# Optimization experiments

Measured on AMD Instinct MI355X. Metric: run time of the kernel, lower is better.

Reference implementation:

```python
import jax, jax.numpy as jnp
import numpy as np

D = 1024
H = 16
HD = D // H
S = 2048
B = 2
FF = 4 * D
EPS = 1e-5
NEG_INF = -100000.0


def setup_inputs() -> dict:
    key = jax.random.key(0)
    ks = jax.random.split(key, 16)
    sd = 0.02
    inp = {
        'x': jax.random.normal(ks[0], (B, S, D), dtype=jnp.float32),
        'Wq': jax.random.normal(ks[1], (D, D), dtype=jnp.float32) * sd,
        'bq': jnp.zeros((D,), jnp.float32),
        'Wk': jax.random.normal(ks[2], (D, D), dtype=jnp.float32) * sd,
        'bk': jnp.zeros((D,), jnp.float32),
        'Wv': jax.random.normal(ks[3], (D, D), dtype=jnp.float32) * sd,
        'bv': jnp.zeros((D,), jnp.float32),
        'Wo': jax.random.normal(ks[4], (D, D), dtype=jnp.float32) * sd,
        'bo': jnp.zeros((D,), jnp.float32),
        'W1': jax.random.normal(ks[5], (D, FF), dtype=jnp.float32) * sd,
        'b1': jnp.zeros((FF,), jnp.float32),
        'W2': jax.random.normal(ks[6], (FF, D), dtype=jnp.float32) * sd,
        'b2': jnp.zeros((D,), jnp.float32),
        'g1': jnp.ones((D,), jnp.float32),
        's1': jnp.zeros((D,), jnp.float32),
        'g2': jnp.ones((D,), jnp.float32),
        's2': jnp.zeros((D,), jnp.float32),
    }
    return inp


def layer_norm(x, scale, shift):
    # torch: (x - mean) / (std + eps), std with Bessel correction (ddof=1)
    mean = jnp.mean(x, axis=-1, keepdims=True)
    std = jnp.std(x, axis=-1, keepdims=True, ddof=1)
    return (x - mean) / (std + EPS) * scale + shift


def attention(x, Wq, bq, Wk, bk, Wv, bv, Wo, bo):
    b, s, d = x.shape
    q = (x @ Wq + bq).reshape(b, s, H, HD).transpose(0, 2, 1, 3)  # [b,h,s,hd]
    k = (x @ Wk + bk).reshape(b, s, H, HD).transpose(0, 2, 1, 3)
    v = (x @ Wv + bv).reshape(b, s, H, HD).transpose(0, 2, 1, 3)
    scores = jnp.einsum('bhqd,bhkd->bhqk', q, k) / jnp.sqrt(jnp.float32(HD))
    mask = jnp.triu(jnp.ones((s, s), bool), k=1)
    scores = jnp.where(mask, NEG_INF, scores)
    attn = jax.nn.softmax(scores, axis=-1)
    ctx = jnp.einsum('bhqk,bhkd->bhqd', attn, v)
    ctx = ctx.transpose(0, 2, 1, 3).reshape(b, s, d)
    return ctx @ Wo + bo


def reference(x, Wq, bq, Wk, bk, Wv, bv, Wo, bo, W1, b1, W2, b2, g1, s1, g2, s2):
    shortcut = x
    h = layer_norm(x, g1, s1)
    h = attention(h, Wq, bq, Wk, bk, Wv, bv, Wo, bo)
    x = shortcut + h  # dropout=0.0 -> identity
    shortcut = x
    h = layer_norm(x, g2, s2)
    h = jax.nn.gelu(h @ W1 + b1, approximate=False) @ W2 + b2
    return h + shortcut
```

## Files before the change

kernel.cpp:

```cpp
#include <hip/hip_runtime.h>
#include <hip/hip_bf16.h>
#include <math.h>

#define D_   1024
#define H_   16
#define HD_  64
#define S_   2048
#define B_   2
#define FF_  4096
#define M_   (B_*S_)
#define QKVN (3*D_)

typedef __bf16 bf16;
typedef bf16 bf16x8 __attribute__((ext_vector_type(8)));
typedef bf16 bf16x4 __attribute__((ext_vector_type(4)));
typedef float f32x4 __attribute__((ext_vector_type(4)));

#define MFMA16(a,b,c) __builtin_amdgcn_mfma_f32_16x16x32_bf16(a,b,c,0,0,0)

__device__ __forceinline__ void gld16(const void* g, void* l) {
    __builtin_amdgcn_global_load_lds(
        (const __attribute__((address_space(1))) void*)g,
        (__attribute__((address_space(3))) void*)l, 16, 0, 0);
}

__global__ __launch_bounds__(256) void transpose_cast(const float* __restrict__ W,
                                                      bf16* __restrict__ WT,
                                                      int K, int N) {
    __shared__ float t[64][65];
    int k0 = blockIdx.x * 64, n0 = blockIdx.y * 64;
    int tid = threadIdx.x;
    int tr = tid >> 4, tc = tid & 15;
    #pragma unroll
    for (int i = 0; i < 4; i++) {
        int r = tr + i * 16;
        float4 v = *(const float4*)&W[(size_t)(k0 + r) * N + n0 + tc * 4];
        t[r][tc * 4 + 0] = v.x; t[r][tc * 4 + 1] = v.y;
        t[r][tc * 4 + 2] = v.z; t[r][tc * 4 + 3] = v.w;
    }
    __syncthreads();
    #pragma unroll
    for (int i = 0; i < 4; i++) {
        int r = tr + i * 16;
        bf16x4 o;
        #pragma unroll
        for (int j = 0; j < 4; j++) o[j] = (bf16)t[tc * 4 + j][r];
        *(bf16x4*)&WT[(size_t)(n0 + r) * K + k0 + tc * 4] = o;
    }
}

__global__ __launch_bounds__(256) void transpose_v(const bf16* __restrict__ qkv,
                                                   bf16* __restrict__ VT) {
    __shared__ __align__(16) bf16 t[64][72];
    int bh = blockIdx.y; int b = bh >> 4, h = bh & 15;
    int s0 = blockIdx.x * 64;
    const bf16* vbase = qkv + (size_t)b * S_ * QKVN + 2048 + h * 64;
    int tid = threadIdx.x;
    #pragma unroll
    for (int i = 0; i < 2; i++) {
        int e = tid + i * 256; int r = e >> 3, cg = e & 7;
        *(bf16x8*)&t[r][cg * 8] = *(const bf16x8*)&vbase[(size_t)(s0 + r) * QKVN + cg * 8];
    }
    __syncthreads();
    #pragma unroll
    for (int i = 0; i < 2; i++) {
        int e = tid + i * 256; int d = e >> 3, cg = e & 7;
        bf16x8 v;
        #pragma unroll
        for (int j = 0; j < 8; j++) v[j] = t[cg * 8 + j][d];
        *(bf16x8*)&VT[((size_t)bh * 64 + d) * S_ + s0 + cg * 8] = v;
    }
}

__global__ void concat3(const float* __restrict__ a, const float* __restrict__ b,
                        const float* __restrict__ c, float* __restrict__ o) {
    int i = blockIdx.x * 256 + threadIdx.x;
    o[i] = (i < 1024) ? a[i] : (i < 2048 ? b[i - 1024] : c[i - 2048]);
}

__global__ __launch_bounds__(256) void ln_kernel(const float* __restrict__ x,
                                                 const float* __restrict__ g,
                                                 const float* __restrict__ sh,
                                                 bf16* __restrict__ out) {
    int row = blockIdx.x * 4 + (threadIdx.x >> 6);
    int lane = threadIdx.x & 63;
    const float4* xr = (const float4*)(x + (size_t)row * D_);
    float4 v[4]; float sum = 0.f, ss = 0.f;
    #pragma unroll
    for (int c = 0; c < 4; c++) {
        v[c] = xr[lane + 64 * c];
        sum += v[c].x + v[c].y + v[c].z + v[c].w;
        ss  += v[c].x * v[c].x + v[c].y * v[c].y + v[c].z * v[c].z + v[c].w * v[c].w;
    }
    #pragma unroll
    for (int o = 32; o; o >>= 1) { sum += __shfl_xor(sum, o); ss += __shfl_xor(ss, o); }
    float mean = sum * (1.f / 1024.f);
    float var  = (ss - 1024.f * mean * mean) * (1.f / 1023.f);
    float inv  = 1.f / (sqrtf(var) + 1e-5f);
    const float4* gp = (const float4*)g;
    const float4* sp = (const float4*)sh;
    bf16x4* op = (bf16x4*)(out + (size_t)row * D_);
    #pragma unroll
    for (int c = 0; c < 4; c++) {
        int idx = lane + 64 * c;
        float4 gv = gp[idx], sv = sp[idx];
        float y0 = (v[c].x - mean) * inv * gv.x + sv.x;
        float y1 = (v[c].y - mean) * inv * gv.y + sv.y;
        float y2 = (v[c].z - mean) * inv * gv.z + sv.z;
        float y3 = (v[c].w - mean) * inv * gv.w + sv.w;
        op[idx] = (bf16x4){(bf16)y0, (bf16)y1, (bf16)y2, (bf16)y3};
    }
}

template<int MODE>
__global__ __launch_bounds__(512, 2) void gemm256(const bf16* __restrict__ A,
                                                  const bf16* __restrict__ BT,
                                                  const float* __restrict__ bias,
                                                  void* __restrict__ outp,
                                                  int M, int N, int K, int KSLICE) {
    __shared__ __align__(16) bf16 a_lds[3 * 256 * 32];
    __shared__ __align__(16) bf16 b_lds[3 * 256 * 32];
    int tid = threadIdx.x, w = tid >> 6, lane = tid & 63;
    int gx = gridDim.x, gxy = gx * gridDim.y;
    int nwg = gxy * gridDim.z;
    int flat = blockIdx.z * gxy + blockIdx.y * gx + blockIdx.x;
    int chunk = nwg >> 3;
    int swz = (flat & 7) * chunk + (flat >> 3);
    int z = swz / gxy, rem = swz - z * gxy;
    int m0 = (rem / gx) * 256, n0 = (rem % gx) * 256;
    int kbase = z * KSLICE;
    int nk = KSLICE >> 5;
    int lr = lane & 15, lh = lane >> 4;
    int wr = w >> 2, wc = w & 3;

    int g0 = w * 64 + lane;
    int row0 = g0 >> 2, cs0 = (g0 & 3) ^ ((row0 >> 1) & 3);
    int g1 = g0 + 512;
    int row1 = g1 >> 2, cs1 = (g1 & 3) ^ ((row1 >> 1) & 3);
    int dst0 = w * 512;
    int dst1 = w * 512 + 4096;

    auto STAGE = [&](int buf, int k0) {
        bf16* ab = a_lds + buf * 8192;
        bf16* bb = b_lds + buf * 8192;
        gld16(&A [(size_t)(m0 + row0) * K + k0 + cs0 * 8], ab + dst0);
        gld16(&A [(size_t)(m0 + row1) * K + k0 + cs1 * 8], ab + dst1);
        gld16(&BT[(size_t)(n0 + row0) * K + k0 + cs0 * 8], bb + dst0);
        gld16(&BT[(size_t)(n0 + row1) * K + k0 + cs1 * 8], bb + dst1);
    };

    f32x4 acc[8][4] = {};
    STAGE(0, kbase);
    STAGE(1, kbase + 32);
    asm volatile("s_waitcnt vmcnt(4)" ::: "memory");
    __builtin_amdgcn_s_barrier();
    __builtin_amdgcn_sched_barrier(0);

    int rchk = (lr >> 1) & 3;
    int fcol = ((lh ^ rchk) * 8);
    for (int kt = 0; kt < nk; ++kt) {
        int b0 = kt % 3;
        const bf16* ab = a_lds + b0 * 8192;
        const bf16* bb = b_lds + b0 * 8192;
        bf16x8 af[8], bf[4];
        #pragma unroll
        for (int m = 0; m < 8; m++)
            af[m] = *(const bf16x8*)&ab[(wr * 128 + m * 16 + lr) * 32 + fcol];
        #pragma unroll
        for (int n = 0; n < 4; n++)
            bf[n] = *(const bf16x8*)&bb[(wc * 64 + n * 16 + lr) * 32 + fcol];
        if (kt + 2 < nk) {
            STAGE((kt + 2) % 3, kbase + (kt + 2) * 32);
            asm volatile("s_waitcnt vmcnt(4)" ::: "memory");
        } else {
            asm volatile("s_waitcnt vmcnt(0)" ::: "memory");
        }
        __builtin_amdgcn_s_setprio(1);
        #pragma unroll
        for (int m = 0; m < 8; m++)
            #pragma unroll
            for (int n = 0; n < 4; n++)
                acc[m][n] = MFMA16(af[m], bf[n], acc[m][n]);
        __builtin_amdgcn_s_setprio(0);
        __builtin_amdgcn_s_barrier();
        __builtin_amdgcn_sched_barrier(0);
    }

    #pragma unroll
    for (int m = 0; m < 8; m++) {
        #pragma unroll
        for (int n = 0; n < 4; n++) {
            int col = n0 + wc * 64 + n * 16 + lr;
            float bv = (MODE == 3) ? 0.f : bias[col];
            #pragma unroll
            for (int r = 0; r < 4; r++) {
                int row = m0 + wr * 128 + m * 16 + lh * 4 + r;
                float vv = acc[m][n][r] + bv;
                if (MODE == 2) vv = 0.5f * vv * (1.f + erff(vv * 0.70710678118654752f));
                if (MODE == 3) ((float*)outp)[((size_t)z * M + row) * N + col] = vv;
                else           ((bf16*)outp)[(size_t)row * N + col] = (bf16)vv;
            }
        }
    }
}

__global__ __launch_bounds__(256) void reduce4(const float* __restrict__ part,
                                               const float* __restrict__ bias,
                                               const float* __restrict__ res,
                                               float* __restrict__ out) {
    int i = blockIdx.x * 256 + threadIdx.x;
    const float4* p = (const float4*)part;
    const size_t s4 = (size_t)M_ * 1024 / 4;
    float4 a = p[i], b = p[i + s4], c = p[i + 2 * s4], d = p[i + 3 * s4];
    float4 bv = ((const float4*)bias)[i & 255];
    float4 rv = ((const float4*)res)[i];
    float4 o;
    o.x = a.x + b.x + c.x + d.x + bv.x + rv.x;
    o.y = a.y + b.y + c.y + d.y + bv.y + rv.y;
    o.z = a.z + b.z + c.z + d.z + bv.z + rv.z;
    o.w = a.w + b.w + c.w + d.w + bv.w + rv.w;
    ((float4*)out)[i] = o;
}

__global__ __launch_bounds__(256) void reduce_ln(const float* __restrict__ part,
                                                 const float* __restrict__ bias,
                                                 const float* __restrict__ res,
                                                 const float* __restrict__ g,
                                                 const float* __restrict__ sh,
                                                 float* __restrict__ x2,
                                                 bf16* __restrict__ h2) {
    __shared__ float s_sum[4], s_ss[4];
    int row = blockIdx.x, t = threadIdx.x;
    int wv = t >> 6, lane = t & 63;
    size_t i = (size_t)row * 256 + t;
    const float4* p = (const float4*)part;
    const size_t s4 = (size_t)M_ * 1024 / 4;
    float4 a = p[i], b = p[i + s4], c = p[i + 2 * s4], d = p[i + 3 * s4];
    float4 bv = ((const float4*)bias)[t];
    float4 rv = ((const float4*)res)[i];
    float4 v;
    v.x = a.x + b.x + c.x + d.x + bv.x + rv.x;
    v.y = a.y + b.y + c.y + d.y + bv.y + rv.y;
    v.z = a.z + b.z + c.z + d.z + bv.z + rv.z;
    v.w = a.w + b.w + c.w + d.w + bv.w + rv.w;
    ((float4*)x2)[i] = v;
    float sum = v.x + v.y + v.z + v.w;
    float ss  = v.x * v.x + v.y * v.y + v.z * v.z + v.w * v.w;
    #pragma unroll
    for (int o = 32; o; o >>= 1) { sum += __shfl_xor(sum, o); ss += __shfl_xor(ss, o); }
    if (lane == 0) { s_sum[wv] = sum; s_ss[wv] = ss; }
    __syncthreads();
    sum = s_sum[0] + s_sum[1] + s_sum[2] + s_sum[3];
    ss  = s_ss[0] + s_ss[1] + s_ss[2] + s_ss[3];
    float mean = sum * (1.f / 1024.f);
    float var  = (ss - 1024.f * mean * mean) * (1.f / 1023.f);
    float inv  = 1.f / (sqrtf(var) + 1e-5f);
    float4 gv = ((const float4*)g)[t], sv = ((const float4*)sh)[t];
    bf16x4 o4;
    o4[0] = (bf16)((v.x - mean) * inv * gv.x + sv.x);
    o4[1] = (bf16)((v.y - mean) * inv * gv.y + sv.y);
    o4[2] = (bf16)((v.z - mean) * inv * gv.z + sv.z);
    o4[3] = (bf16)((v.w - mean) * inv * gv.w + sv.w);
    *(bf16x4*)&h2[(size_t)row * D_ + t * 4] = o4;
}

__global__ __launch_bounds__(256) void attn_kernel(const bf16* __restrict__ qkv,
                                                   const bf16* __restrict__ VT,
                                                   bf16* __restrict__ ctx) {
    __shared__ __align__(16) bf16 k_lds[64 * 72];
    __shared__ __align__(16) bf16 vt_lds[64 * 72];
    __shared__ __align__(16) bf16 p_lds[4 * 16 * 72];
    int bh = blockIdx.x; int b = bh >> 4, h = bh & 15;
    int qt = gridDim.y - 1 - blockIdx.y;
    int q0 = qt * 64;
    int tid = threadIdx.x, w = tid >> 6, lane = tid & 63;
    int lr = lane & 15, lh = lane >> 4;
    const size_t RS = QKVN;
    const bf16* qbase = qkv + (size_t)b * S_ * RS + h * 64;
    const bf16* kbase = qbase + 1024;
    const bf16* vtb = VT + (size_t)bh * 64 * S_;

    int qrow = q0 + w * 16 + lr;
    bf16x8 aq[2];
    #pragma unroll
    for (int dc = 0; dc < 2; dc++) {
        bf16x8 t8 = *(const bf16x8*)&qbase[(size_t)qrow * RS + dc * 32 + lh * 8];
        #pragma unroll
        for (int j = 0; j < 8; j++) t8[j] = (bf16)((float)t8[j] * 0.125f);
        aq[dc] = t8;
    }

    f32x4 o_acc[4] = {};
    float mrow[4], lrow[4];
    #pragma unroll
    for (int r = 0; r < 4; r++) { mrow[r] = -1e30f; lrow[r] = 0.f; }

    int er = tid >> 3, ecg = tid & 7;
    int ntile = qt + 1;
    bf16x8 kreg0 = *(const bf16x8*)&kbase[(size_t)er * RS + ecg * 8];
    bf16x8 kreg1 = *(const bf16x8*)&kbase[(size_t)(er + 32) * RS + ecg * 8];
    bf16x8 vreg0 = *(const bf16x8*)&vtb[(size_t)er * S_ + ecg * 8];
    bf16x8 vreg1 = *(const bf16x8*)&vtb[(size_t)(er + 32) * S_ + ecg * 8];

    for (int t = 0; t < ntile; t++) {
        int kv0 = t * 64;
        *(bf16x8*)&k_lds [er * 72 + ecg * 8]        = kreg0;
        *(bf16x8*)&k_lds [(er + 32) * 72 + ecg * 8] = kreg1;
        *(bf16x8*)&vt_lds[er * 72 + ecg * 8]        = vreg0;
        *(bf16x8*)&vt_lds[(er + 32) * 72 + ecg * 8] = vreg1;
        __syncthreads();
        if (t + 1 < ntile) {
            int kn = kv0 + 64;
            kreg0 = *(const bf16x8*)&kbase[(size_t)(kn + er) * RS + ecg * 8];
            kreg1 = *(const bf16x8*)&kbase[(size_t)(kn + er + 32) * RS + ecg * 8];
            vreg0 = *(const bf16x8*)&vtb[(size_t)er * S_ + kn + ecg * 8];
            vreg1 = *(const bf16x8*)&vtb[(size_t)(er + 32) * S_ + kn + ecg * 8];
        }

        f32x4 sc[4] = {};
        #pragma unroll
        for (int kf = 0; kf < 4; kf++)
            #pragma unroll
            for (int dc = 0; dc < 2; dc++) {
                bf16x8 bk = *(const bf16x8*)&k_lds[(kf * 16 + lr) * 72 + dc * 32 + lh * 8];
                sc[kf] = MFMA16(aq[dc], bk, sc[kf]);
            }

        if (t == ntile - 1) {
            #pragma unroll
            for (int kf = 0; kf < 4; kf++) {
                int kvg = kv0 + kf * 16 + lr;
                #pragma unroll
                for (int r = 0; r < 4; r++) {
                    int qg = q0 + w * 16 + lh * 4 + r;
                    if (kvg > qg) sc[kf][r] = -100000.0f;
                }
            }
        }

        float pmax[4];
        #pragma unroll
        for (int r = 0; r < 4; r++)
            pmax[r] = fmaxf(fmaxf(sc[0][r], sc[1][r]), fmaxf(sc[2][r], sc[3][r]));
        #pragma unroll
        for (int o = 1; o < 16; o <<= 1)
            #pragma unroll
            for (int r = 0; r < 4; r++)
                pmax[r] = fmaxf(pmax[r], __shfl_xor(pmax[r], o));

        bool ok = true;
        #pragma unroll
        for (int r = 0; r < 4; r++) ok = ok && (pmax[r] <= mrow[r] + 8.f);
        if (!__all(ok)) {
            #pragma unroll
            for (int r = 0; r < 4; r++) {
                float mn = fmaxf(mrow[r], pmax[r]);
                float s = __expf(mrow[r] - mn);
                mrow[r] = mn;
                lrow[r] *= s;
                #pragma unroll
                for (int df = 0; df < 4; df++) o_acc[df][r] *= s;
            }
        }

        float psum[4] = {0.f, 0.f, 0.f, 0.f};
        #pragma unroll
        for (int kf = 0; kf < 4; kf++)
            #pragma unroll
            for (int r = 0; r < 4; r++) {
                float p = __expf(sc[kf][r] - mrow[r]);
                sc[kf][r] = p;
                psum[r] += p;
            }
        #pragma unroll
        for (int o = 1; o < 16; o <<= 1)
            #pragma unroll
            for (int r = 0; r < 4; r++) psum[r] += __shfl_xor(psum[r], o);
        #pragma unroll
        for (int r = 0; r < 4; r++) lrow[r] += psum[r];

        bf16* pw = &p_lds[w * 16 * 72];
        #pragma unroll
        for (int kf = 0; kf < 4; kf++)
            #pragma unroll
            for (int r = 0; r < 4; r++)
                pw[(lh * 4 + r) * 72 + kf * 16 + lr] = (bf16)sc[kf][r];
        asm volatile("s_waitcnt lgkmcnt(0)" ::: "memory");
        __builtin_amdgcn_sched_barrier(0);
        bf16x8 ap[2];
        ap[0] = *(const bf16x8*)&pw[lr * 72 + lh * 8];
        ap[1] = *(const bf16x8*)&pw[lr * 72 + 32 + lh * 8];
        #pragma unroll
        for (int df = 0; df < 4; df++) {
            #pragma unroll
            for (int kc = 0; kc < 2; kc++) {
                bf16x8 bv = *(const bf16x8*)&vt_lds[(df * 16 + lr) * 72 + kc * 32 + lh * 8];
                o_acc[df] = MFMA16(ap[kc], bv, o_acc[df]);
            }
        }
        __syncthreads();
    }

    #pragma unroll
    for (int df = 0; df < 4; df++)
        #pragma unroll
        for (int r = 0; r < 4; r++) {
            int row = q0 + w * 16 + lh * 4 + r;
            int col = h * 64 + df * 16 + lr;
            ctx[((size_t)b * S_ + row) * D_ + col] = (bf16)(o_acc[df][r] / lrow[r]);
        }
}

extern "C" void kernel_launch(void* const* d_in, const int* in_sizes, int n_in,
                              void* d_out, int out_size, void* d_ws, size_t ws_size,
                              hipStream_t stream) {
    const float* x  = (const float*)d_in[0];
    const float* Wq = (const float*)d_in[1];
    const float* bq = (const float*)d_in[2];
    const float* Wk = (const float*)d_in[3];
    const float* bk = (const float*)d_in[4];
    const float* Wv = (const float*)d_in[5];
    const float* bv = (const float*)d_in[6];
    const float* Wo = (const float*)d_in[7];
    const float* bo = (const float*)d_in[8];
    const float* W1 = (const float*)d_in[9];
    const float* b1 = (const float*)d_in[10];
    const float* W2 = (const float*)d_in[11];
    const float* b2 = (const float*)d_in[12];
    const float* g1 = (const float*)d_in[13];
    const float* s1 = (const float*)d_in[14];
    const float* g2 = (const float*)d_in[15];
    const float* s2 = (const float*)d_in[16];
    float* out = (float*)d_out;

    char* ws = (char*)d_ws;
    size_t off = 0;
    auto alloc = [&](size_t bytes) -> char* {
        char* p = ws + off; off += (bytes + 255) & ~(size_t)255; return p;
    };
    bf16*  wt_qkv = (bf16*)alloc((size_t)QKVN * D_ * 2);
    bf16*  wt_o   = (bf16*)alloc((size_t)D_ * D_ * 2);
    bf16*  wt_1   = (bf16*)alloc((size_t)FF_ * D_ * 2);
    bf16*  wt_2   = (bf16*)alloc((size_t)D_ * FF_ * 2);
    float* qkvb   = (float*)alloc((size_t)QKVN * 4);
    bf16*  h1     = (bf16*)alloc((size_t)M_ * D_ * 2);
    bf16*  qkv    = (bf16*)alloc((size_t)M_ * QKVN * 2);
    bf16*  vtbuf  = (bf16*)alloc((size_t)M_ * D_ * 2);
    bf16*  ctx    = (bf16*)alloc((size_t)M_ * D_ * 2);
    float* x2     = (float*)alloc((size_t)M_ * D_ * 4);
    bf16*  h2     = (bf16*)alloc((size_t)M_ * D_ * 2);
    bf16*  gbuf   = (bf16*)alloc((size_t)M_ * FF_ * 2);
    float* part   = (float*)alloc((size_t)4 * M_ * D_ * 4);

    transpose_cast<<<dim3(16, 16), 256, 0, stream>>>(Wq, wt_qkv, D_, D_);
    transpose_cast<<<dim3(16, 16), 256, 0, stream>>>(Wk, wt_qkv + (size_t)D_ * D_, D_, D_);
    transpose_cast<<<dim3(16, 16), 256, 0, stream>>>(Wv, wt_qkv + (size_t)2 * D_ * D_, D_, D_);
    transpose_cast<<<dim3(16, 16), 256, 0, stream>>>(Wo, wt_o, D_, D_);
    transpose_cast<<<dim3(16, 64), 256, 0, stream>>>(W1, wt_1, D_, FF_);
    transpose_cast<<<dim3(64, 16), 256, 0, stream>>>(W2, wt_2, FF_, D_);
    concat3<<<12, 256, 0, stream>>>(bq, bk, bv, qkvb);

    ln_kernel<<<M_ / 4, 256, 0, stream>>>(x, g1, s1, h1);
    gemm256<0><<<dim3(QKVN / 256, M_ / 256, 1), 512, 0, stream>>>(h1, wt_qkv, qkvb, qkv, M_, QKVN, D_, D_);
    transpose_v<<<dim3(S_ / 64, B_ * H_), 256, 0, stream>>>(qkv, vtbuf);
    attn_kernel<<<dim3(B_ * H_, S_ / 64), 256, 0, stream>>>(qkv, vtbuf, ctx);
    gemm256<3><<<dim3(D_ / 256, M_ / 256, 4), 512, 0, stream>>>(ctx, wt_o, nullptr, part, M_, D_, D_, D_ / 4);
    reduce_ln<<<M_, 256, 0, stream>>>(part, bo, x, g2, s2, x2, h2);
    gemm256<2><<<dim3(FF_ / 256, M_ / 256, 1), 512, 0, stream>>>(h2, wt_1, b1, gbuf, M_, FF_, D_, D_);
    gemm256<3><<<dim3(D_ / 256, M_ / 256, 4), 512, 0, stream>>>(gbuf, wt_2, nullptr, part, M_, D_, FF_, FF_ / 4);
    reduce4<<<(M_ * D_) / 1024, 256, 0, stream>>>(part, b2, x2, out);
}
```

Before: 387.3 us.

## Compute transposed attention scores so P stays in registers, dropping LDS round-trip

Swaps the MFMA operands so the score tile is computed transposed (keys by queries). Each lane then owns one query row, so the row max and sum need only two cross-lane shuffles, and softmax state shrinks to scalars. The probabilities are packed straight into the B operand for the PV MFMA instead of going through an LDS scratch buffer. To match, the V^T tile is stored into LDS with a permuted column order, and the output is written as vectorized bf16x4 stores. The risk is that the permuted V layout is subtle, and any mismatch with the MFMA k-ordering would break correctness. It also only touches the attention kernel, which is one part of the whole layer.

```diff
diff --git a/kernel.cpp b/kernel.cpp
--- a/kernel.cpp
+++ b/kernel.cpp
@@ -269,7 +269,6 @@
                                                    bf16* __restrict__ ctx) {
     __shared__ __align__(16) bf16 k_lds[64 * 72];
     __shared__ __align__(16) bf16 vt_lds[64 * 72];
-    __shared__ __align__(16) bf16 p_lds[4 * 16 * 72];
     int bh = blockIdx.x; int b = bh >> 4, h = bh & 15;
     int qt = gridDim.y - 1 - blockIdx.y;
     int q0 = qt * 64;
@@ -290,12 +289,14 @@
         aq[dc] = t8;
     }
 
-    f32x4 o_acc[4] = {};
-    float mrow[4], lrow[4];
-    #pragma unroll
-    for (int r = 0; r < 4; r++) { mrow[r] = -1e30f; lrow[r] = 0.f; }
+    f32x4 oT[4] = {};
+    float mrow = -1e30f, lrow = 0.f;
 
     int er = tid >> 3, ecg = tid & 7;
+    int o0 = ecg * 2, o1 = o0 + 1;
+    int p0 = (o0 & 8) + 2 * (o0 & 3) + ((o0 >> 2) & 1);
+    int p1 = (o1 & 8) + 2 * (o1 & 3) + ((o1 >> 2) & 1);
+
     int ntile = qt + 1;
     bf16x8 kreg0 = *(const bf16x8*)&kbase[(size_t)er * RS + ecg * 8];
     bf16x8 kreg1 = *(const bf16x8*)&kbase[(size_t)(er + 32) * RS + ecg * 8];
@@ -304,10 +305,18 @@
 
     for (int t = 0; t < ntile; t++) {
         int kv0 = t * 64;
-        *(bf16x8*)&k_lds [er * 72 + ecg * 8]        = kreg0;
-        *(bf16x8*)&k_lds [(er + 32) * 72 + ecg * 8] = kreg1;
-        *(bf16x8*)&vt_lds[er * 72 + ecg * 8]        = vreg0;
-        *(bf16x8*)&vt_lds[(er + 32) * 72 + ecg * 8] = vreg1;
+        *(bf16x8*)&k_lds[er * 72 + ecg * 8]        = kreg0;
+        *(bf16x8*)&k_lds[(er + 32) * 72 + ecg * 8] = kreg1;
+        {
+            bf16x4 lo0 = {vreg0[0], vreg0[1], vreg0[2], vreg0[3]};
+            bf16x4 hi0 = {vreg0[4], vreg0[5], vreg0[6], vreg0[7]};
+            bf16x4 lo1 = {vreg1[0], vreg1[1], vreg1[2], vreg1[3]};
+            bf16x4 hi1 = {vreg1[4], vreg1[5], vreg1[6], vreg1[7]};
+            *(bf16x4*)&vt_lds[er * 72 + p0 * 4]        = lo0;
+            *(bf16x4*)&vt_lds[er * 72 + p1 * 4]        = hi0;
+            *(bf16x4*)&vt_lds[(er + 32) * 72 + p0 * 4] = lo1;
+            *(bf16x4*)&vt_lds[(er + 32) * 72 + p1 * 4] = hi1;
+        }
         __syncthreads();
         if (t + 1 < ntile) {
             int kn = kv0 + 64;
@@ -322,93 +331,81 @@
         for (int kf = 0; kf < 4; kf++)
             #pragma unroll
             for (int dc = 0; dc < 2; dc++) {
-                bf16x8 bk = *(const bf16x8*)&k_lds[(kf * 16 + lr) * 72 + dc * 32 + lh * 8];
-                sc[kf] = MFMA16(aq[dc], bk, sc[kf]);
+                bf16x8 ak = *(const bf16x8*)&k_lds[(kf * 16 + lr) * 72 + dc * 32 + lh * 8];
+                sc[kf] = MFMA16(ak, aq[dc], sc[kf]);
             }
 
         if (t == ntile - 1) {
-            #pragma unroll
-            for (int kf = 0; kf < 4; kf++) {
-                int kvg = kv0 + kf * 16 + lr;
+            int qg = q0 + w * 16 + lr;
+            #pragma unroll
+            for (int kf = 0; kf < 4; kf++)
                 #pragma unroll
                 for (int r = 0; r < 4; r++) {
-                    int qg = q0 + w * 16 + lh * 4 + r;
+                    int kvg = kv0 + kf * 16 + lh * 4 + r;
                     if (kvg > qg) sc[kf][r] = -100000.0f;
                 }
+        }
+
+        float pmax = sc[0][0];
+        #pragma unroll
+        for (int kf = 0; kf < 4; kf++)
+            #pragma unroll
+            for (int r = 0; r < 4; r++) pmax = fmaxf(pmax, sc[kf][r]);
+        pmax = fmaxf(pmax, __shfl_xor(pmax, 16));
+        pmax = fmaxf(pmax, __shfl_xor(pmax, 32));
+
+        if (!__all(pmax <= mrow + 8.f)) {
+            float mn = fmaxf(mrow, pmax);
+            float s = __expf(mrow - mn);
+            mrow = mn;
+            lrow *= s;
+            #pragma unroll
+            for (int df = 0; df < 4; df++)
+                #pragma unroll
+                for (int r = 0; r < 4; r++) oT[df][r] *= s;
+        }
+
+        float psum = 0.f;
+        #pragma unroll
+        for (int kf = 0; kf < 4; kf++)
+            #pragma unroll
+            for (int r = 0; r < 4; r++) {
+                float p = __expf(sc[kf][r] - mrow);
+                sc[kf][r] = p;
+                psum += p;
             }
-        }
-
-        float pmax[4];
-        #pragma unroll
-        for (int r = 0; r < 4; r++)
-            pmax[r] = fmaxf(fmaxf(sc[0][r], sc[1][r]), fmaxf(sc[2][r], sc[3][r]));
-        #pragma unroll
-        for (int o = 1; o < 16; o <<= 1)
-            #pragma unroll
-            for (int r = 0; r < 4; r++)
-                pmax[r] = fmaxf(pmax[r], __shfl_xor(pmax[r], o));
-
-        bool ok = true;
-        #pragma unroll
-        for (int r = 0; r < 4; r++) ok = ok && (pmax[r] <= mrow[r] + 8.f);
-        if (!__all(ok)) {
-            #pragma unroll
-            for (int r = 0; r < 4; r++) {
-                float mn = fmaxf(mrow[r], pmax[r]);
-                float s = __expf(mrow[r] - mn);
-                mrow[r] = mn;
-                lrow[r] *= s;
-                #pragma unroll
-                for (int df = 0; df < 4; df++) o_acc[df][r] *= s;
-            }
-        }
-
-        float psum[4] = {0.f, 0.f, 0.f, 0.f};
-        #pragma unroll
-        for (int kf = 0; kf < 4; kf++)
-            #pragma unroll
-            for (int r = 0; r < 4; r++) {
-                float p = __expf(sc[kf][r] - mrow[r]);
-                sc[kf][r] = p;
-                psum[r] += p;
-            }
-        #pragma unroll
-        for (int o = 1; o < 16; o <<= 1)
-            #pragma unroll
-            for (int r = 0; r < 4; r++) psum[r] += __shfl_xor(psum[r], o);
-        #pragma unroll
-        for (int r = 0; r < 4; r++) lrow[r] += psum[r];
-
-        bf16* pw = &p_lds[w * 16 * 72];
-        #pragma unroll
-        for (int kf = 0; kf < 4; kf++)
-            #pragma unroll
-            for (int r = 0; r < 4; r++)
-                pw[(lh * 4 + r) * 72 + kf * 16 + lr] = (bf16)sc[kf][r];
-        asm volatile("s_waitcnt lgkmcnt(0)" ::: "memory");
-        __builtin_amdgcn_sched_barrier(0);
-        bf16x8 ap[2];
-        ap[0] = *(const bf16x8*)&pw[lr * 72 + lh * 8];
-        ap[1] = *(const bf16x8*)&pw[lr * 72 + 32 + lh * 8];
+        psum += __shfl_xor(psum, 16);
+        psum += __shfl_xor(psum, 32);
+        lrow += psum;
+
+        bf16x8 pb0, pb1;
+        #pragma unroll
+        for (int r = 0; r < 4; r++) {
+            pb0[r]     = (bf16)sc[0][r];
+            pb0[4 + r] = (bf16)sc[1][r];
+            pb1[r]     = (bf16)sc[2][r];
+            pb1[4 + r] = (bf16)sc[3][r];
+        }
+
         #pragma unroll
         for (int df = 0; df < 4; df++) {
-            #pragma unroll
-            for (int kc = 0; kc < 2; kc++) {
-                bf16x8 bv = *(const bf16x8*)&vt_lds[(df * 16 + lr) * 72 + kc * 32 + lh * 8];
-                o_acc[df] = MFMA16(ap[kc], bv, o_acc[df]);
-            }
+            bf16x8 av0 = *(const bf16x8*)&vt_lds[(df * 16 + lr) * 72 + lh * 8];
+            bf16x8 av1 = *(const bf16x8*)&vt_lds[(df * 16 + lr) * 72 + 32 + lh * 8];
+            oT[df] = MFMA16(av0, pb0, oT[df]);
+            oT[df] = MFMA16(av1, pb1, oT[df]);
         }
         __syncthreads();
     }
 
-    #pragma unroll
-    for (int df = 0; df < 4; df++)
-        #pragma unroll
-        for (int r = 0; r < 4; r++) {
-            int row = q0 + w * 16 + lh * 4 + r;
-            int col = h * 64 + df * 16 + lr;
-            ctx[((size_t)b * S_ + row) * D_ + col] = (bf16)(o_acc[df][r] / lrow[r]);
-        }
+    float inv = 1.f / lrow;
+    int orow = q0 + w * 16 + lr;
+    #pragma unroll
+    for (int df = 0; df < 4; df++) {
+        bf16x4 o4;
+        #pragma unroll
+        for (int r = 0; r < 4; r++) o4[r] = (bf16)(oT[df][r] * inv);
+        *(bf16x4*)&ctx[((size_t)b * S_ + orow) * D_ + h * 64 + df * 16 + lh * 4] = o4;
+    }
 }
 
 extern "C" void kernel_launch(void* const* d_in, const int* in_sizes, int n_in,
```

Result: faster. 373.4 us (-3.6%).
